# Kernel optimization log

Measured on AMD Instinct MI355X. Metric: run time of the kernel, lower is better.

Reference implementation:

```python
import jax, jax.numpy as jnp
import numpy as np

N_NODES = 100000
N_EDGES = 1600000
D = 32  # atom and bond feature dim


def _mlp(x, W1, b1, W2, b2, W3, b3):
    # fff: Linear(in,128) -> ReLU -> Linear(128,64) -> ReLU -> Linear(64,32)
    h = jax.nn.relu(x @ W1 + b1)
    h = jax.nn.relu(h @ W2 + b2)
    return h @ W3 + b3


def _init_mlp(key, in_dim):
    ks = jax.random.split(key, 3)
    def lin(k, fan_in, fan_out):
        bound = 1.0 / np.sqrt(fan_in)
        kw, kb = jax.random.split(k)
        W = jax.random.uniform(kw, (fan_in, fan_out), jnp.float32, -bound, bound)
        b = jax.random.uniform(kb, (fan_out,), jnp.float32, -bound, bound)
        return W, b
    W1, b1 = lin(ks[0], in_dim, 128)
    W2, b2 = lin(ks[1], 128, 64)
    W3, b3 = lin(ks[2], 64, 32)
    return W1, b1, W2, b2, W3, b3


def setup_inputs() -> dict:
    key = jax.random.key(0)
    k_bonds, k_a1, k_a2, k_atoms, k_e, k_v = jax.random.split(key, 6)
    inp = {
        "bonds": jax.random.normal(k_bonds, (N_EDGES, D), jnp.float32),
        "bond_atom_1": jax.random.randint(k_a1, (N_EDGES,), 0, N_NODES, jnp.int64),
        "bond_atom_2": jax.random.randint(k_a2, (N_EDGES,), 0, N_NODES, jnp.int64),
        "atoms": jax.random.normal(k_atoms, (N_NODES, D), jnp.float32),
    }
    We1, be1, We2, be2, We3, be3 = _init_mlp(k_e, 96)
    Wv1, bv1, Wv2, bv2, Wv3, bv3 = _init_mlp(k_v, 64)
    inp.update(We1=We1, be1=be1, We2=We2, be2=be2, We3=We3, be3=be3,
               Wv1=Wv1, bv1=bv1, Wv2=Wv2, bv2=bv2, Wv3=Wv3, bv3=bv3)
    return inp


def reference(bonds, bond_atom_1, bond_atom_2, atoms,
              We1, be1, We2, be2, We3, be3,
              Wv1, bv1, Wv2, bv2, Wv3, bv3):
    # Edge update: gather endpoint atom features, concat with bond feats, MLP
    atom1 = atoms[bond_atom_1]                    # [E, D]
    atom2 = atoms[bond_atom_2]                    # [E, D]
    e_in = jnp.concatenate([atom1, atom2, bonds], axis=1)  # [E, 3D]
    new_bonds = _mlp(e_in, We1, be1, We2, be2, We3, be3)    # [E, 32]

    # Node update: scatter-mean new bond features onto target atoms
    # (PyG default flow aggregates messages at edge_index[1] == bond_atom_2)
    n = atoms.shape[0]
    seg_sum = jax.ops.segment_sum(new_bonds, bond_atom_2, num_segments=n)
    counts = jax.ops.segment_sum(jnp.ones((new_bonds.shape[0],), new_bonds.dtype),
                                 bond_atom_2, num_segments=n)
    mean_bonds = seg_sum / jnp.maximum(counts, 1.0)[:, None]  # [N, 32]

    v_in = jnp.concatenate([mean_bonds, atoms], axis=1)        # [N, 64]
    new_atoms = _mlp(v_in, Wv1, bv1, Wv2, bv2, Wv3, bv3)       # [N, 32]
    return (new_atoms, new_bonds)
```

## Files before the change

kernel.cpp:

```cpp
#include <hip/hip_runtime.h>
#include <hip/hip_bf16.h>

#define NN 100000
#define NE 1600000
#define NB_SCAN 391
#define ETILES 12500
#define EGRID 512
#define NGRID 1024

typedef __attribute__((ext_vector_type(8))) short bfrag8;
typedef __attribute__((ext_vector_type(4))) float f32x4;
typedef __attribute__((ext_vector_type(8))) unsigned short us8;
typedef __attribute__((ext_vector_type(4))) unsigned int u32x4;

__device__ __forceinline__ unsigned short f2bf(float f) {
  unsigned int u = __float_as_uint(f);
  u += 0x7fffu + ((u >> 16) & 1u);
  return (unsigned short)(u >> 16);
}

__device__ __forceinline__ unsigned int pk2(float a, float b) {
  unsigned int r;
  asm("v_cvt_pk_bf16_f32 %0, %1, %2" : "=v"(r) : "v"(a), "v"(b));
  return r;
}

__device__ __forceinline__ uint2 pk4(float v0, float v1, float v2, float v3) {
  return make_uint2(pk2(v0, v1), pk2(v2, v3));
}

__device__ __forceinline__ bfrag8 pack8(float4 a, float4 b) {
  union { u32x4 u; bfrag8 f; } c;
  c.u[0] = pk2(a.x, a.y); c.u[1] = pk2(a.z, a.w);
  c.u[2] = pk2(b.x, b.y); c.u[3] = pk2(b.z, b.w);
  return c.f;
}

__device__ __forceinline__ bfrag8 as_frag(us8 v) {
  union { us8 u; bfrag8 f; } c;
  c.u = v;
  return c.f;
}

__device__ __forceinline__ float bl(unsigned int u) { return __uint_as_float(u << 16); }
__device__ __forceinline__ float bh(unsigned int u) { return __uint_as_float(u & 0xffff0000u); }

__device__ __forceinline__ f32x4 mfma16(bfrag8 a, bfrag8 b, f32x4 c) {
  return __builtin_amdgcn_mfma_f32_16x16x32_bf16(a, b, c, 0, 0, 0);
}

__device__ __forceinline__ void gload_lds16(const void* g, void* l) {
  __builtin_amdgcn_global_load_lds(
      (const __attribute__((address_space(1))) unsigned int*)g,
      (__attribute__((address_space(3))) unsigned int*)l, 16, 0, 0);
}

__global__ void prep(const float* __restrict__ atoms, unsigned short* __restrict__ atoms_bf,
                     const int* __restrict__ a2, int* __restrict__ cnt,
                     const float* __restrict__ We1, const float* __restrict__ We2,
                     const float* __restrict__ We3, const float* __restrict__ Wv1,
                     const float* __restrict__ Wv2, const float* __restrict__ Wv3,
                     unsigned short* __restrict__ wp) {
  const int b = blockIdx.x, tid = threadIdx.x;
  if (b < 3125) {
    const int i = b * 256 + tid;
    float4 v = *(const float4*)(atoms + (size_t)i * 4);
    *(uint2*)(atoms_bf + (size_t)i * 4) = pk4(v.x, v.y, v.z, v.w);
  } else if (b < 3125 + 6250) {
    const int e = (b - 3125) * 256 + tid;
    if (e < NE) atomicAdd(&cnt[a2[e]], 1);
  } else {
    const int i = (b - 9375) * 256 + tid;
    const float* src; int base, K, N;
    if (i < 12288)      { src = We1; base = 0;     K = 96;  N = 128; }
    else if (i < 20480) { src = We2; base = 12288; K = 128; N = 64;  }
    else if (i < 22528) { src = We3; base = 20480; K = 64;  N = 32;  }
    else if (i < 30720) { src = Wv1; base = 22528; K = 64;  N = 128; }
    else if (i < 38912) { src = Wv2; base = 30720; K = 128; N = 64;  }
    else                { src = Wv3; base = 38912; K = 64;  N = 32;  }
    const int il = i - base;
    const int j = il & 7, gc = il >> 3;
    const int c = gc % N, g = gc / N;
    wp[i] = f2bf(src[(g * 8 + j) * N + c]);
    (void)K;
  }
}

__global__ void scan_blocks(const int* __restrict__ cnt, int* __restrict__ off,
                            int* __restrict__ bsum) {
  __shared__ int s[256];
  const int t = threadIdx.x;
  const int idx = blockIdx.x * 256 + t;
  int v = (idx < NN) ? cnt[idx] : 0;
  s[t] = v;
  __syncthreads();
  for (int d = 1; d < 256; d <<= 1) {
    int x = (t >= d) ? s[t - d] : 0;
    __syncthreads();
    s[t] += x;
    __syncthreads();
  }
  if (idx < NN) off[idx] = s[t] - v;
  if (t == 255) bsum[blockIdx.x] = s[255];
}

__global__ void scan_finalize(int* __restrict__ off, const int* __restrict__ bsum,
                              int* __restrict__ cursor) {
  __shared__ int red[256];
  const int b = blockIdx.x, t = threadIdx.x;
  int s = 0;
  for (int k = t; k < b; k += 256) s += bsum[k];
  red[t] = s;
  __syncthreads();
  for (int d = 128; d > 0; d >>= 1) {
    if (t < d) red[t] += red[t + d];
    __syncthreads();
  }
  const int base = red[0];
  const int idx = b * 256 + t;
  if (idx < NN) {
    int o = off[idx] + base;
    off[idx] = o;
    cursor[idx] = o;
  }
  if (idx == 0) off[NN] = NE;
}

__global__ void fill_k(const int* __restrict__ a2, int* __restrict__ cursor,
                       int* __restrict__ buf, int mode) {
  int e = blockIdx.x * 256 + threadIdx.x;
  if (e < NE) {
    int p = atomicAdd(&cursor[a2[e]], 1);
    if (mode) buf[e] = p;
    else buf[p] = e;
  }
}

__global__ __launch_bounds__(256, 2) void edge_kernel(
    const float* __restrict__ bonds, const int* __restrict__ a1p, const int* __restrict__ a2p,
    const unsigned short* __restrict__ atoms_bf,
    const float* __restrict__ be1, const float* __restrict__ be2, const float* __restrict__ be3,
    const unsigned short* __restrict__ wpack,
    float* __restrict__ new_bonds,
    const int* __restrict__ pos, unsigned short* __restrict__ nb_bf) {
  __shared__ unsigned short sW[22528];
  __shared__ float sB1[128], sB2[64], sB3[32];
  __shared__ unsigned short sH1[128 * 136];

  const int tid = threadIdx.x;
  const int lane = tid & 63, wv = tid >> 6;
  const int cl = lane & 15, q = lane >> 4;
  const int esub = wv * 32 + cl;

  {
    const char* src = (const char*)wpack;
    char* dst = (char*)sW;
#pragma unroll
    for (int i = 0; i < 11; ++i) {
      const int c = i * 4 + wv;
      gload_lds16(src + c * 1024 + lane * 16, dst + c * 1024);
    }
  }
  if (tid < 128) sB1[tid] = be1[tid];
  else if (tid < 192) sB2[tid - 128] = be2[tid - 128];
  else if (tid < 224) sB3[tid - 192] = be3[tid - 192];

  int tile = blockIdx.x;
  us8 ra1[2], ra2[2];
  float4 rb[2][2];
  int ia1n[2], ia2n[2];

#pragma unroll
  for (int t = 0; t < 2; ++t) {
    const int e = tile * 128 + esub + t * 16;
    const int ia1 = a1p[e], ia2 = a2p[e];
    ra1[t] = *(const us8*)(atoms_bf + (size_t)ia1 * 32 + q * 8);
    ra2[t] = *(const us8*)(atoms_bf + (size_t)ia2 * 32 + q * 8);
    const float* bp = bonds + (size_t)e * 32 + q * 8;
    rb[t][0] = *(const float4*)(bp);
    rb[t][1] = *(const float4*)(bp + 4);
  }
  {
    int tn = tile + EGRID; if (tn >= ETILES) tn = tile;
#pragma unroll
    for (int t = 0; t < 2; ++t) {
      const int e = tn * 128 + esub + t * 16;
      ia1n[t] = a1p[e]; ia2n[t] = a2p[e];
    }
  }
  __syncthreads();

  for (; tile < ETILES; tile += EGRID) {
    bfrag8 xb0[2], xb1[2], xb2[2];
#pragma unroll
    for (int t = 0; t < 2; ++t) {
      xb0[t] = as_frag(ra1[t]);
      xb1[t] = as_frag(ra2[t]);
      xb2[t] = pack8(rb[t][0], rb[t][1]);
    }
    int posc[2] = {0, 0};
    if (nb_bf) {
#pragma unroll
      for (int t = 0; t < 2; ++t) posc[t] = pos[tile * 128 + esub + t * 16];
    }
    const int tn = (tile + EGRID < ETILES) ? tile + EGRID : tile;
#pragma unroll
    for (int t = 0; t < 2; ++t) {
      ra1[t] = *(const us8*)(atoms_bf + (size_t)ia1n[t] * 32 + q * 8);
      ra2[t] = *(const us8*)(atoms_bf + (size_t)ia2n[t] * 32 + q * 8);
      const int e = tn * 128 + esub + t * 16;
      const float* bp = bonds + (size_t)e * 32 + q * 8;
      rb[t][0] = *(const float4*)(bp);
      rb[t][1] = *(const float4*)(bp + 4);
    }
    {
      int tnn = tile + 2 * EGRID; if (tnn >= ETILES) tnn = tn;
#pragma unroll
      for (int t = 0; t < 2; ++t) {
        const int e = tnn * 128 + esub + t * 16;
        ia1n[t] = a1p[e]; ia2n[t] = a2p[e];
      }
    }

#pragma unroll
    for (int rt = 0; rt < 8; ++rt) {
      const unsigned short* wa = &sW[(q * 128 + rt * 16 + cl) * 8];
      bfrag8 w0 = *(const bfrag8*)(wa);
      bfrag8 w1 = *(const bfrag8*)(wa + 4096);
      bfrag8 w2 = *(const bfrag8*)(wa + 8192);
      f32x4 acc[2];
      acc[0] = (f32x4){0.f, 0.f, 0.f, 0.f};
      acc[1] = (f32x4){0.f, 0.f, 0.f, 0.f};
#pragma unroll
      for (int t = 0; t < 2; ++t) {
        acc[t] = mfma16(w0, xb0[t], acc[t]);
        acc[t] = mfma16(w1, xb1[t], acc[t]);
        acc[t] = mfma16(w2, xb2[t], acc[t]);
      }
      const int c0 = rt * 16 + q * 4;
#pragma unroll
      for (int t = 0; t < 2; ++t) {
        uint2 hv = pk4(fmaxf(acc[t][0] + sB1[c0 + 0], 0.f),
                       fmaxf(acc[t][1] + sB1[c0 + 1], 0.f),
                       fmaxf(acc[t][2] + sB1[c0 + 2], 0.f),
                       fmaxf(acc[t][3] + sB1[c0 + 3], 0.f));
        *(uint2*)&sH1[(esub + t * 16) * 136 + c0] = hv;
      }
    }
    __syncthreads();

    bfrag8 hb[4][2];
#pragma unroll
    for (int t = 0; t < 2; ++t) {
      const unsigned short* hr = &sH1[(esub + t * 16) * 136 + q * 8];
#pragma unroll
      for (int ks = 0; ks < 4; ++ks) hb[ks][t] = *(const bfrag8*)(hr + ks * 32);
    }
    __syncthreads();

    unsigned short* sH2 = sH1;
#pragma unroll
    for (int rt = 0; rt < 4; ++rt) {
      f32x4 acc[2];
      acc[0] = (f32x4){0.f, 0.f, 0.f, 0.f};
      acc[1] = (f32x4){0.f, 0.f, 0.f, 0.f};
#pragma unroll
      for (int ks = 0; ks < 4; ++ks) {
        bfrag8 w = *(const bfrag8*)&sW[12288 + ks * 2048 + (q * 64 + rt * 16 + cl) * 8];
#pragma unroll
        for (int t = 0; t < 2; ++t) acc[t] = mfma16(w, hb[ks][t], acc[t]);
      }
      const int c0 = rt * 16 + q * 4;
#pragma unroll
      for (int t = 0; t < 2; ++t) {
        uint2 hv = pk4(fmaxf(acc[t][0] + sB2[c0 + 0], 0.f),
                       fmaxf(acc[t][1] + sB2[c0 + 1], 0.f),
                       fmaxf(acc[t][2] + sB2[c0 + 2], 0.f),
                       fmaxf(acc[t][3] + sB2[c0 + 3], 0.f));
        *(uint2*)&sH2[(esub + t * 16) * 72 + c0] = hv;
      }
    }
    __syncthreads();

    bfrag8 gb0[2], gb1[2];
#pragma unroll
    for (int t = 0; t < 2; ++t) {
      const unsigned short* hr = &sH2[(esub + t * 16) * 72 + q * 8];
      gb0[t] = *(const bfrag8*)(hr);
      gb1[t] = *(const bfrag8*)(hr + 32);
    }
#pragma unroll
    for (int rt = 0; rt < 2; ++rt) {
      bfrag8 w0 = *(const bfrag8*)&sW[20480 + (q * 32 + rt * 16 + cl) * 8];
      bfrag8 w1 = *(const bfrag8*)&sW[20480 + 1024 + (q * 32 + rt * 16 + cl) * 8];
      const int c0 = rt * 16 + q * 4;
#pragma unroll
      for (int t = 0; t < 2; ++t) {
        f32x4 acc = {0.f, 0.f, 0.f, 0.f};
        acc = mfma16(w0, gb0[t], acc);
        acc = mfma16(w1, gb1[t], acc);
        const int e = tile * 128 + esub + t * 16;
        float4 o;
        o.x = acc[0] + sB3[c0 + 0];
        o.y = acc[1] + sB3[c0 + 1];
        o.z = acc[2] + sB3[c0 + 2];
        o.w = acc[3] + sB3[c0 + 3];
        *(float4*)(new_bonds + (size_t)e * 32 + c0) = o;
        if (nb_bf) {
          *(uint2*)(nb_bf + (size_t)posc[t] * 32 + c0) =
              make_uint2(pk2(o.x, o.y), pk2(o.z, o.w));
        }
      }
    }
    __syncthreads();
  }
}

__global__ __launch_bounds__(256, 8) void gather_seq(
    const int* __restrict__ off, const unsigned short* __restrict__ nb_bf,
    unsigned short* __restrict__ mean_bf) {
  const int gt = blockIdx.x * 256 + threadIdx.x;
  const int n = gt >> 3, sl = gt & 7;
  const int o0 = off[n], o1 = off[n + 1];
  const int deg = o1 - o0;
  float s0 = 0.f, s1 = 0.f, s2 = 0.f, s3 = 0.f;
  const unsigned short* p = nb_bf + (size_t)o0 * 32 + sl * 4;
  int i = 0;
  for (; i + 1 < deg; i += 2) {
    uint2 a = *(const uint2*)(p);
    uint2 b = *(const uint2*)(p + 32);
    p += 64;
    s0 += bl(a.x) + bl(b.x); s1 += bh(a.x) + bh(b.x);
    s2 += bl(a.y) + bl(b.y); s3 += bh(a.y) + bh(b.y);
  }
  if (i < deg) {
    uint2 a = *(const uint2*)(p);
    s0 += bl(a.x); s1 += bh(a.x); s2 += bl(a.y); s3 += bh(a.y);
  }
  const float inv = 1.0f / fmaxf((float)deg, 1.0f);
  *(uint2*)(mean_bf + (size_t)n * 32 + sl * 4) =
      make_uint2(pk2(s0 * inv, s1 * inv), pk2(s2 * inv, s3 * inv));
}

__global__ __launch_bounds__(256, 8) void gather_rand(
    const int* __restrict__ off, const int* __restrict__ csr,
    const float* __restrict__ new_bonds, float* __restrict__ mean_f32) {
  const int tid = blockIdx.x * 256 + threadIdx.x;
  const int n = tid >> 3, sl = tid & 7;
  const int o0 = off[n], o1 = off[n + 1];
  float4 s0 = {0.f, 0.f, 0.f, 0.f}, s1 = {0.f, 0.f, 0.f, 0.f};
  int i = o0;
  for (; i + 1 < o1; i += 2) {
    const int ea = csr[i], eb = csr[i + 1];
    float4 a = *(const float4*)(new_bonds + (size_t)ea * 32 + sl * 4);
    float4 b = *(const float4*)(new_bonds + (size_t)eb * 32 + sl * 4);
    s0.x += a.x; s0.y += a.y; s0.z += a.z; s0.w += a.w;
    s1.x += b.x; s1.y += b.y; s1.z += b.z; s1.w += b.w;
  }
  if (i < o1) {
    const int ea = csr[i];
    float4 a = *(const float4*)(new_bonds + (size_t)ea * 32 + sl * 4);
    s0.x += a.x; s0.y += a.y; s0.z += a.z; s0.w += a.w;
  }
  const float inv = 1.0f / fmaxf((float)(o1 - o0), 1.0f);
  float4 m;
  m.x = (s0.x + s1.x) * inv;
  m.y = (s0.y + s1.y) * inv;
  m.z = (s0.z + s1.z) * inv;
  m.w = (s0.w + s1.w) * inv;
  *(float4*)(mean_f32 + (size_t)n * 32 + sl * 4) = m;
}

template <int MODE>
__global__ __launch_bounds__(256, 4) void node_mlp(
    const unsigned short* __restrict__ atoms_bf,
    const float* __restrict__ bv1, const float* __restrict__ bv2, const float* __restrict__ bv3,
    const unsigned short* __restrict__ wpack,
    const void* __restrict__ mean_src, float* __restrict__ new_atoms) {
  __shared__ unsigned short sW[18432];
  __shared__ float sB1[128], sB2[64], sB3[32];
  __shared__ unsigned short sV[64 * 72];
  __shared__ unsigned short sH1[64 * 136];

  const int tid = threadIdx.x;
  const int lane = tid & 63, wv = tid >> 6;
  const int cl = lane & 15, q = lane >> 4;
  const int nl = tid >> 2, l4 = tid & 3;

  {
    const uint4* src = (const uint4*)wpack;
    uint4* dst = (uint4*)sW;
#pragma unroll
    for (int i = 0; i < 9; ++i) dst[tid + i * 256] = src[tid + i * 256];
  }
  if (tid < 128) sB1[tid] = bv1[tid];
  if (tid < 64) sB2[tid] = bv2[tid];
  if (tid < 32) sB3[tid] = bv3[tid];

  for (int n0 = blockIdx.x * 64; n0 < NN; n0 += NGRID * 64) {
    __syncthreads();

    {
      const int n = n0 + nl;
      if (n < NN) {
        if (l4 < 2) {
          if (MODE == 1) {
            const unsigned short* mp = (const unsigned short*)mean_src + (size_t)n * 32 + l4 * 16;
            *(us8*)&sV[nl * 72 + l4 * 16] = *(const us8*)(mp);
            *(us8*)&sV[nl * 72 + l4 * 16 + 8] = *(const us8*)(mp + 8);
          } else {
            const float* sp = (const float*)mean_src + (size_t)n * 32 + l4 * 16;
            float4 a = *(const float4*)(sp);
            float4 b = *(const float4*)(sp + 4);
            float4 c = *(const float4*)(sp + 8);
            float4 d = *(const float4*)(sp + 12);
            uint4 o0, o1;
            o0.x = pk2(a.x, a.y); o0.y = pk2(a.z, a.w);
            o0.z = pk2(b.x, b.y); o0.w = pk2(b.z, b.w);
            o1.x = pk2(c.x, c.y); o1.y = pk2(c.z, c.w);
            o1.z = pk2(d.x, d.y); o1.w = pk2(d.z, d.w);
            *(uint4*)&sV[nl * 72 + l4 * 16] = o0;
            *(uint4*)&sV[nl * 72 + l4 * 16 + 8] = o1;
          }
        } else {
          const unsigned short* ap = atoms_bf + (size_t)n * 32 + (l4 - 2) * 16;
          *(us8*)&sV[nl * 72 + 32 + (l4 - 2) * 16] = *(const us8*)(ap);
          *(us8*)&sV[nl * 72 + 32 + (l4 - 2) * 16 + 8] = *(const us8*)(ap + 8);
        }
      } else {
        us8 z = {0, 0, 0, 0, 0, 0, 0, 0};
        *(us8*)&sV[nl * 72 + l4 * 16] = z;
        *(us8*)&sV[nl * 72 + l4 * 16 + 8] = z;
      }
    }
    __syncthreads();

    const int nt = wv * 16;
    const int ng = n0 + nt + cl;

    bfrag8 vb0 = *(const bfrag8*)&sV[(nt + cl) * 72 + q * 8];
    bfrag8 vb1 = *(const bfrag8*)&sV[(nt + cl) * 72 + 32 + q * 8];
#pragma unroll
    for (int rt = 0; rt < 8; ++rt) {
      f32x4 acc = {0.f, 0.f, 0.f, 0.f};
      acc = mfma16(*(const bfrag8*)&sW[(q * 128 + rt * 16 + cl) * 8], vb0, acc);
      acc = mfma16(*(const bfrag8*)&sW[4096 + (q * 128 + rt * 16 + cl) * 8], vb1, acc);
      const int c0 = rt * 16 + q * 4;
      uint2 hv = pk4(fmaxf(acc[0] + sB1[c0 + 0], 0.f),
                     fmaxf(acc[1] + sB1[c0 + 1], 0.f),
                     fmaxf(acc[2] + sB1[c0 + 2], 0.f),
                     fmaxf(acc[3] + sB1[c0 + 3], 0.f));
      *(uint2*)&sH1[(nt + cl) * 136 + c0] = hv;
    }
    __syncthreads();

    bfrag8 hb[4];
    {
      const unsigned short* hr = &sH1[(nt + cl) * 136 + q * 8];
#pragma unroll
      for (int ks = 0; ks < 4; ++ks) hb[ks] = *(const bfrag8*)(hr + ks * 32);
    }
    __syncthreads();
#pragma unroll
    for (int rt = 0; rt < 4; ++rt) {
      f32x4 acc = {0.f, 0.f, 0.f, 0.f};
#pragma unroll
      for (int ks = 0; ks < 4; ++ks)
        acc = mfma16(*(const bfrag8*)&sW[8192 + ks * 2048 + (q * 64 + rt * 16 + cl) * 8], hb[ks], acc);
      const int c0 = rt * 16 + q * 4;
      uint2 hv = pk4(fmaxf(acc[0] + sB2[c0 + 0], 0.f),
                     fmaxf(acc[1] + sB2[c0 + 1], 0.f),
                     fmaxf(acc[2] + sB2[c0 + 2], 0.f),
                     fmaxf(acc[3] + sB2[c0 + 3], 0.f));
      *(uint2*)&sV[(nt + cl) * 72 + c0] = hv;
    }
    __syncthreads();

    bfrag8 gb0 = *(const bfrag8*)&sV[(nt + cl) * 72 + q * 8];
    bfrag8 gb1 = *(const bfrag8*)&sV[(nt + cl) * 72 + 32 + q * 8];
    if (ng < NN) {
      float* outp = new_atoms + (size_t)ng * 32;
#pragma unroll
      for (int rt = 0; rt < 2; ++rt) {
        f32x4 acc = {0.f, 0.f, 0.f, 0.f};
        acc = mfma16(*(const bfrag8*)&sW[16384 + (q * 32 + rt * 16 + cl) * 8], gb0, acc);
        acc = mfma16(*(const bfrag8*)&sW[16384 + 1024 + (q * 32 + rt * 16 + cl) * 8], gb1, acc);
        const int c0 = rt * 16 + q * 4;
        float4 o;
        o.x = acc[0] + sB3[c0 + 0];
        o.y = acc[1] + sB3[c0 + 1];
        o.z = acc[2] + sB3[c0 + 2];
        o.w = acc[3] + sB3[c0 + 3];
        *(float4*)(outp + c0) = o;
      }
    }
  }
}

extern "C" void kernel_launch(void* const* d_in, const int* in_sizes, int n_in,
                              void* d_out, int out_size, void* d_ws, size_t ws_size,
                              hipStream_t stream) {
  const float* bonds = (const float*)d_in[0];
  const int* a1 = (const int*)d_in[1];
  const int* a2 = (const int*)d_in[2];
  const float* atoms = (const float*)d_in[3];
  const float* We1 = (const float*)d_in[4];
  const float* be1 = (const float*)d_in[5];
  const float* We2 = (const float*)d_in[6];
  const float* be2 = (const float*)d_in[7];
  const float* We3 = (const float*)d_in[8];
  const float* be3 = (const float*)d_in[9];
  const float* Wv1 = (const float*)d_in[10];
  const float* bv1 = (const float*)d_in[11];
  const float* Wv2 = (const float*)d_in[12];
  const float* bv2 = (const float*)d_in[13];
  const float* Wv3 = (const float*)d_in[14];
  const float* bv3 = (const float*)d_in[15];

  float* out = (float*)d_out;
  float* new_atoms = out;
  float* new_bonds = out + (size_t)NN * 32;

  char* ws = (char*)d_ws;
  int* cnt    = (int*)(ws + 0);
  int* off    = (int*)(ws + 400000);
  int* bsum   = (int*)(ws + 800016);
  unsigned short* wp = (unsigned short*)(ws + 802064);
  int* poscsr = (int*)(ws + 883984);
  unsigned short* atoms_bf = (unsigned short*)(ws + 7283984);
  unsigned short* mean_bf  = (unsigned short*)(ws + 13683984);
  unsigned short* nb_bf    = (unsigned short*)(ws + 20083984);

  const int fast = (ws_size >= (size_t)122483984) ? 1 : 0;

  hipMemsetAsync(cnt, 0, (size_t)NN * 4, stream);

  prep<<<9535, 256, 0, stream>>>(atoms, atoms_bf, a2, cnt,
                                 We1, We2, We3, Wv1, Wv2, Wv3, wp);

  scan_blocks<<<NB_SCAN, 256, 0, stream>>>(cnt, off, bsum);
  scan_finalize<<<NB_SCAN, 256, 0, stream>>>(off, bsum, cnt);
  fill_k<<<(NE + 255) / 256, 256, 0, stream>>>(a2, cnt, poscsr, fast);

  edge_kernel<<<EGRID, 256, 0, stream>>>(bonds, a1, a2, atoms_bf, be1, be2, be3, wp,
                                         new_bonds, poscsr, fast ? nb_bf : nullptr);

  if (fast) {
    gather_seq<<<NN * 8 / 256, 256, 0, stream>>>(off, nb_bf, mean_bf);
    node_mlp<1><<<NGRID, 256, 0, stream>>>(atoms_bf, bv1, bv2, bv3, wp + 22528,
                                           mean_bf, new_atoms);
  } else {
    gather_rand<<<NN * 8 / 256, 256, 0, stream>>>(off, poscsr, new_bonds, new_atoms);
    node_mlp<0><<<NGRID, 256, 0, stream>>>(atoms_bf, bv1, bv2, bv3, wp + 22528,
                                           new_atoms, new_atoms);
  }
}
```

Before: 394.7 us.

## Process edges in CSR order so bf16 bond writes are sequential

In the fast path the edge kernel now walks edges in destination-sorted (CSR) order through an edge-id permutation. The bf16 copy of the new bond features is therefore written contiguously instead of scattered by position, and edges that share a target atom are handled together. In exchange, the fp32 bond loads and new_bonds stores become scattered by edge id, and one more level of index prefetch is added. fill_k now always writes the edge permutation, and the edge kernel is templated on the path.

New measurement: 445.5 us. 12.9% more time.

```diff
diff --git a/kernel.cpp b/kernel.cpp
--- a/kernel.cpp
+++ b/kernel.cpp
@@ -71,18 +71,17 @@
     if (e < NE) atomicAdd(&cnt[a2[e]], 1);
   } else {
     const int i = (b - 9375) * 256 + tid;
-    const float* src; int base, K, N;
-    if (i < 12288)      { src = We1; base = 0;     K = 96;  N = 128; }
-    else if (i < 20480) { src = We2; base = 12288; K = 128; N = 64;  }
-    else if (i < 22528) { src = We3; base = 20480; K = 64;  N = 32;  }
-    else if (i < 30720) { src = Wv1; base = 22528; K = 64;  N = 128; }
-    else if (i < 38912) { src = Wv2; base = 30720; K = 128; N = 64;  }
-    else                { src = Wv3; base = 38912; K = 64;  N = 32;  }
+    const float* src; int base, N;
+    if (i < 12288)      { src = We1; base = 0;     N = 128; }
+    else if (i < 20480) { src = We2; base = 12288; N = 64;  }
+    else if (i < 22528) { src = We3; base = 20480; N = 32;  }
+    else if (i < 30720) { src = Wv1; base = 22528; N = 128; }
+    else if (i < 38912) { src = Wv2; base = 30720; N = 64;  }
+    else                { src = Wv3; base = 38912; N = 32;  }
     const int il = i - base;
     const int j = il & 7, gc = il >> 3;
     const int c = gc % N, g = gc / N;
     wp[i] = f2bf(src[(g * 8 + j) * N + c]);
-    (void)K;
   }
 }
 
@@ -127,22 +126,22 @@
 }
 
 __global__ void fill_k(const int* __restrict__ a2, int* __restrict__ cursor,
-                       int* __restrict__ buf, int mode) {
+                       int* __restrict__ csr) {
   int e = blockIdx.x * 256 + threadIdx.x;
   if (e < NE) {
     int p = atomicAdd(&cursor[a2[e]], 1);
-    if (mode) buf[e] = p;
-    else buf[p] = e;
-  }
-}
-
+    csr[p] = e;
+  }
+}
+
+template <int FAST>
 __global__ __launch_bounds__(256, 2) void edge_kernel(
     const float* __restrict__ bonds, const int* __restrict__ a1p, const int* __restrict__ a2p,
     const unsigned short* __restrict__ atoms_bf,
     const float* __restrict__ be1, const float* __restrict__ be2, const float* __restrict__ be3,
     const unsigned short* __restrict__ wpack,
     float* __restrict__ new_bonds,
-    const int* __restrict__ pos, unsigned short* __restrict__ nb_bf) {
+    const int* __restrict__ csr, unsigned short* __restrict__ nb_bf) {
   __shared__ unsigned short sW[22528];
   __shared__ float sB1[128], sB2[64], sB3[32];
   __shared__ unsigned short sH1[128 * 136];
@@ -166,27 +165,34 @@
   else if (tid < 224) sB3[tid - 192] = be3[tid - 192];
 
   int tile = blockIdx.x;
+  int ec[2], en[2], enn[2];
+  int ia1n[2], ia2n[2];
   us8 ra1[2], ra2[2];
   float4 rb[2][2];
-  int ia1n[2], ia2n[2];
-
+
+  {
+    int tn = tile + EGRID; if (tn >= ETILES) tn = tile;
+    int tnn = tile + 2 * EGRID; if (tnn >= ETILES) tnn = tn;
+#pragma unroll
+    for (int t = 0; t < 2; ++t) {
+      const int s0 = tile * 128 + esub + t * 16;
+      const int s1 = tn * 128 + esub + t * 16;
+      const int s2 = tnn * 128 + esub + t * 16;
+      ec[t] = FAST ? csr[s0] : s0;
+      en[t] = FAST ? csr[s1] : s1;
+      enn[t] = FAST ? csr[s2] : s2;
+    }
+  }
 #pragma unroll
   for (int t = 0; t < 2; ++t) {
-    const int e = tile * 128 + esub + t * 16;
-    const int ia1 = a1p[e], ia2 = a2p[e];
-    ra1[t] = *(const us8*)(atoms_bf + (size_t)ia1 * 32 + q * 8);
-    ra2[t] = *(const us8*)(atoms_bf + (size_t)ia2 * 32 + q * 8);
-    const float* bp = bonds + (size_t)e * 32 + q * 8;
+    const int i1 = a1p[ec[t]], i2 = a2p[ec[t]];
+    ra1[t] = *(const us8*)(atoms_bf + (size_t)i1 * 32 + q * 8);
+    ra2[t] = *(const us8*)(atoms_bf + (size_t)i2 * 32 + q * 8);
+    const float* bp = bonds + (size_t)ec[t] * 32 + q * 8;
     rb[t][0] = *(const float4*)(bp);
     rb[t][1] = *(const float4*)(bp + 4);
-  }
-  {
-    int tn = tile + EGRID; if (tn >= ETILES) tn = tile;
-#pragma unroll
-    for (int t = 0; t < 2; ++t) {
-      const int e = tn * 128 + esub + t * 16;
-      ia1n[t] = a1p[e]; ia2n[t] = a2p[e];
-    }
+    ia1n[t] = a1p[en[t]];
+    ia2n[t] = a2p[en[t]];
   }
   __syncthreads();
 
@@ -198,27 +204,26 @@
       xb1[t] = as_frag(ra2[t]);
       xb2[t] = pack8(rb[t][0], rb[t][1]);
     }
-    int posc[2] = {0, 0};
-    if (nb_bf) {
-#pragma unroll
-      for (int t = 0; t < 2; ++t) posc[t] = pos[tile * 128 + esub + t * 16];
-    }
-    const int tn = (tile + EGRID < ETILES) ? tile + EGRID : tile;
 #pragma unroll
     for (int t = 0; t < 2; ++t) {
       ra1[t] = *(const us8*)(atoms_bf + (size_t)ia1n[t] * 32 + q * 8);
       ra2[t] = *(const us8*)(atoms_bf + (size_t)ia2n[t] * 32 + q * 8);
-      const int e = tn * 128 + esub + t * 16;
-      const float* bp = bonds + (size_t)e * 32 + q * 8;
+      const float* bp = bonds + (size_t)en[t] * 32 + q * 8;
       rb[t][0] = *(const float4*)(bp);
       rb[t][1] = *(const float4*)(bp + 4);
     }
+#pragma unroll
+    for (int t = 0; t < 2; ++t) {
+      ia1n[t] = a1p[enn[t]];
+      ia2n[t] = a2p[enn[t]];
+    }
+    int ennn[2];
     {
-      int tnn = tile + 2 * EGRID; if (tnn >= ETILES) tnn = tn;
+      int t3 = tile + 3 * EGRID; if (t3 >= ETILES) t3 = tile;
 #pragma unroll
       for (int t = 0; t < 2; ++t) {
-        const int e = tnn * 128 + esub + t * 16;
-        ia1n[t] = a1p[e]; ia2n[t] = a2p[e];
+        const int s3 = t3 * 128 + esub + t * 16;
+        ennn[t] = FAST ? csr[s3] : s3;
       }
     }
 
@@ -299,18 +304,24 @@
         f32x4 acc = {0.f, 0.f, 0.f, 0.f};
         acc = mfma16(w0, gb0[t], acc);
         acc = mfma16(w1, gb1[t], acc);
-        const int e = tile * 128 + esub + t * 16;
         float4 o;
         o.x = acc[0] + sB3[c0 + 0];
         o.y = acc[1] + sB3[c0 + 1];
         o.z = acc[2] + sB3[c0 + 2];
         o.w = acc[3] + sB3[c0 + 3];
-        *(float4*)(new_bonds + (size_t)e * 32 + c0) = o;
-        if (nb_bf) {
-          *(uint2*)(nb_bf + (size_t)posc[t] * 32 + c0) =
+        *(float4*)(new_bonds + (size_t)ec[t] * 32 + c0) = o;
+        if (FAST) {
+          const int s = tile * 128 + esub + t * 16;
+          *(uint2*)(nb_bf + (size_t)s * 32 + c0) =
               make_uint2(pk2(o.x, o.y), pk2(o.z, o.w));
         }
       }
+    }
+#pragma unroll
+    for (int t = 0; t < 2; ++t) {
+      ec[t] = en[t];
+      en[t] = enn[t];
+      enn[t] = ennn[t];
     }
     __syncthreads();
   }
@@ -526,7 +537,7 @@
   int* off    = (int*)(ws + 400000);
   int* bsum   = (int*)(ws + 800016);
   unsigned short* wp = (unsigned short*)(ws + 802064);
-  int* poscsr = (int*)(ws + 883984);
+  int* csr    = (int*)(ws + 883984);
   unsigned short* atoms_bf = (unsigned short*)(ws + 7283984);
   unsigned short* mean_bf  = (unsigned short*)(ws + 13683984);
   unsigned short* nb_bf    = (unsigned short*)(ws + 20083984);
@@ -540,17 +551,18 @@
 
   scan_blocks<<<NB_SCAN, 256, 0, stream>>>(cnt, off, bsum);
   scan_finalize<<<NB_SCAN, 256, 0, stream>>>(off, bsum, cnt);
-  fill_k<<<(NE + 255) / 256, 256, 0, stream>>>(a2, cnt, poscsr, fast);
-
-  edge_kernel<<<EGRID, 256, 0, stream>>>(bonds, a1, a2, atoms_bf, be1, be2, be3, wp,
-                                         new_bonds, poscsr, fast ? nb_bf : nullptr);
+  fill_k<<<(NE + 255) / 256, 256, 0, stream>>>(a2, cnt, csr);
 
   if (fast) {
+    edge_kernel<1><<<EGRID, 256, 0, stream>>>(bonds, a1, a2, atoms_bf, be1, be2, be3, wp,
+                                              new_bonds, csr, nb_bf);
     gather_seq<<<NN * 8 / 256, 256, 0, stream>>>(off, nb_bf, mean_bf);
     node_mlp<1><<<NGRID, 256, 0, stream>>>(atoms_bf, bv1, bv2, bv3, wp + 22528,
                                            mean_bf, new_atoms);
   } else {
-    gather_rand<<<NN * 8 / 256, 256, 0, stream>>>(off, poscsr, new_bonds, new_atoms);
+    edge_kernel<0><<<EGRID, 256, 0, stream>>>(bonds, a1, a2, atoms_bf, be1, be2, be3, wp,
+                                              new_bonds, csr, nullptr);
+    gather_rand<<<NN * 8 / 256, 256, 0, stream>>>(off, csr, new_bonds, new_atoms);
     node_mlp<0><<<NGRID, 256, 0, stream>>>(atoms_bf, bv1, bv2, bv3, wp + 22528,
                                            new_atoms, new_atoms);
   }
```
